# Kernel optimization log

Hardware: AMD Instinct MI355X
Metric: run time of the kernel (lower is better)

Reference implementation:

```python
import jax, jax.numpy as jnp
import numpy as np

DIM = 768
HEADS = 12
DIM_HEAD = DIM // HEADS  # 64
INNER = DIM_HEAD * HEADS  # 768
HIDDEN = 4 * DIM  # 3072
N = 31  # num_patches + 1, fixed by Block (num_patches=30)
B = 512
EPS = 1e-5
MASK_VAL = -987654321.0


def layernorm(x, g, b):
    mu = jnp.mean(x, axis=-1, keepdims=True)
    var = jnp.mean(jnp.square(x - mu), axis=-1, keepdims=True)
    return (x - mu) * jax.lax.rsqrt(var + EPS) * g + b


def setup_inputs() -> dict:
    key = jax.random.key(0)
    ks = jax.random.split(key, 12)
    s = 0.02
    return {
        "x": jax.random.normal(ks[0], (B, N, DIM), jnp.float32),
        "ln1_g": jnp.ones((DIM,), jnp.float32),
        "ln1_b": jnp.zeros((DIM,), jnp.float32),
        "w_qkv": jax.random.normal(ks[1], (DIM, 3 * INNER), jnp.float32) * s,
        "scale": jnp.full((HEADS,), DIM_HEAD ** -0.5, jnp.float32),
        "w_o": jax.random.normal(ks[2], (INNER, DIM), jnp.float32) * s,
        "b_o": jnp.zeros((DIM,), jnp.float32),
        "ln2_g": jnp.ones((DIM,), jnp.float32),
        "ln2_b": jnp.zeros((DIM,), jnp.float32),
        "w1": jax.random.normal(ks[3], (DIM, HIDDEN), jnp.float32) * s,
        "b1": jnp.zeros((HIDDEN,), jnp.float32),
        "w2": jax.random.normal(ks[4], (HIDDEN, DIM), jnp.float32) * s,
        "b2": jnp.zeros((DIM,), jnp.float32),
    }


def reference(x, ln1_g, ln1_b, w_qkv, scale, w_o, b_o, ln2_g, ln2_b, w1, b1, w2, b2):
    b, n, _ = x.shape
    # --- LSA attention ---
    h = layernorm(x, ln1_g, ln1_b)
    qkv = h @ w_qkv  # [b, n, 3*inner]
    q, k, v = jnp.split(qkv, 3, axis=-1)
    def split_heads(t):
        return t.reshape(b, n, HEADS, DIM_HEAD).transpose(0, 2, 1, 3)  # b h n d
    q, k, v = split_heads(q), split_heads(k), split_heads(v)
    dots = jnp.einsum('bhid,bhjd->bhij', q, k) * scale[None, :, None, None]
    # diagonal exclusion mask (self-token masked out)
    diag = jnp.eye(n, dtype=bool)
    dots = jnp.where(diag[None, None], MASK_VAL, dots)
    attn = jax.nn.softmax(dots, axis=-1)
    out = jnp.einsum('bhij,bhjd->bhid', attn, v)
    out = out.transpose(0, 2, 1, 3).reshape(b, n, INNER)
    x = x + out @ w_o + b_o
    # --- MLP ---
    h2 = layernorm(x, ln2_g, ln2_b)
    h2 = jax.nn.gelu(h2 @ w1 + b1, approximate=False)
    x = x + h2 @ w2 + b2
    return x
```

## Files before the change

### kernel.cpp

```cpp
#include <hip/hip_runtime.h>
#include <math.h>

#define DIM 768
#define HEADS 12
#define DHEAD 64
#define NTOK 31
#define BATCH 512
#define MTOK (BATCH * NTOK)
#define HIDDEN 3072
#define QKVN 2304
#define MASK_VAL -987654321.0f

typedef short s16x8 __attribute__((ext_vector_type(8)));
typedef float f32x4 __attribute__((ext_vector_type(4)));

static __device__ __forceinline__ float bs2f(unsigned short u) {
  unsigned int x = ((unsigned int)u) << 16;
  return __builtin_bit_cast(float, x);
}
static __device__ __forceinline__ unsigned short f2bs(float f) {
  unsigned int x = __builtin_bit_cast(unsigned int, f);
  x += 0x7fffu + ((x >> 16) & 1u);
  return (unsigned short)(x >> 16);
}

static __device__ __forceinline__ void gload16(const unsigned short* g, unsigned short* l) {
  __builtin_amdgcn_global_load_lds(
      (const __attribute__((address_space(1))) unsigned int*)g,
      (__attribute__((address_space(3))) unsigned int*)l, 16, 0, 0);
}

static __device__ __forceinline__ float epi_apply(int EPI, float v, int col, size_t idx,
                                                  const float* bias, const void* resid) {
  if (EPI == 0) return v;
  if (EPI == 2) {
    float t = v + bias[col];
    float arg = 1.5957691216f * t * (1.f + 0.044715f * t * t);
    return t * __builtin_amdgcn_rcpf(1.f + __expf(-arg));
  }
  if (EPI == 3) return v + bias[col] + ((const float*)resid)[idx];
  return v + bias[col] + bs2f(((const unsigned short*)resid)[idx]);
}

static __device__ __forceinline__ void epi_store(int EPI, void* outp, size_t idx, float t) {
  if (EPI == 4) ((float*)outp)[idx] = t;
  else ((unsigned short*)outp)[idx] = f2bs(t);
}

__global__ __launch_bounds__(256) void transpose_all_kernel(
    const float* __restrict__ w_qkv, const float* __restrict__ w_o,
    const float* __restrict__ w1, const float* __restrict__ w2,
    unsigned short* __restrict__ wqkvT, unsigned short* __restrict__ woT,
    unsigned short* __restrict__ w1T, unsigned short* __restrict__ w2T) {
  int t = blockIdx.x;
  const float* w;
  unsigned short* wt;
  int K, N, tx;
  if (t < 432) { w = w_qkv; wt = wqkvT; K = DIM; N = QKVN; tx = QKVN / 64; }
  else if (t < 576) { t -= 432; w = w_o; wt = woT; K = DIM; N = DIM; tx = DIM / 64; }
  else if (t < 1152) { t -= 576; w = w1; wt = w1T; K = DIM; N = HIDDEN; tx = HIDDEN / 64; }
  else { t -= 1152; w = w2; wt = w2T; K = HIDDEN; N = DIM; tx = DIM / 64; }
  int n0 = (t % tx) * 64, k0 = (t / tx) * 64;

  __shared__ float tl[64][65];
  int tid = threadIdx.x;
  int r = tid >> 4, c4 = (tid & 15) * 4;
#pragma unroll
  for (int i = 0; i < 4; ++i) {
    float4 v = *(const float4*)(w + (size_t)(k0 + r + i * 16) * N + n0 + c4);
    tl[r + i * 16][c4] = v.x;
    tl[r + i * 16][c4 + 1] = v.y;
    tl[r + i * 16][c4 + 2] = v.z;
    tl[r + i * 16][c4 + 3] = v.w;
  }
  __syncthreads();
#pragma unroll
  for (int i = 0; i < 4; ++i) {
    int n = r + i * 16;
    ushort4 o;
    o.x = f2bs(tl[c4 + 0][n]);
    o.y = f2bs(tl[c4 + 1][n]);
    o.z = f2bs(tl[c4 + 2][n]);
    o.w = f2bs(tl[c4 + 3][n]);
    *(ushort4*)(wt + (size_t)(n0 + n) * K + k0 + c4) = o;
  }
}

__global__ __launch_bounds__(256) void ln_kernel(const float* __restrict__ x,
                                                 const float* __restrict__ g,
                                                 const float* __restrict__ bta,
                                                 unsigned short* __restrict__ out) {
  int wid = threadIdx.x >> 6, lane = threadIdx.x & 63;
  size_t row = (size_t)blockIdx.x * 4 + wid;
  const float4* xr = (const float4*)(x + row * DIM);
  float4 v[3];
  v[0] = xr[lane];
  v[1] = xr[lane + 64];
  v[2] = xr[lane + 128];
  float s = 0.f, sq = 0.f;
#pragma unroll
  for (int i = 0; i < 3; ++i) {
    s += v[i].x + v[i].y + v[i].z + v[i].w;
    sq += v[i].x * v[i].x + v[i].y * v[i].y + v[i].z * v[i].z + v[i].w * v[i].w;
  }
#pragma unroll
  for (int off = 32; off; off >>= 1) {
    s += __shfl_xor(s, off);
    sq += __shfl_xor(sq, off);
  }
  float mu = s * (1.f / DIM);
  float var = sq * (1.f / DIM) - mu * mu;
  float rs = rsqrtf(var + 1e-5f);
#pragma unroll
  for (int i = 0; i < 3; ++i) {
    int col = i * 256 + lane * 4;
    float4 gg = *(const float4*)(g + col);
    float4 bb = *(const float4*)(bta + col);
    ushort4 o;
    o.x = f2bs((v[i].x - mu) * rs * gg.x + bb.x);
    o.y = f2bs((v[i].y - mu) * rs * gg.y + bb.y);
    o.z = f2bs((v[i].z - mu) * rs * gg.z + bb.z);
    o.w = f2bs((v[i].w - mu) * rs * gg.w + bb.w);
    *(ushort4*)(out + row * DIM + col) = o;
  }
}

__global__ __launch_bounds__(256) void ln_bf16_kernel(const unsigned short* __restrict__ x,
                                                      const float* __restrict__ g,
                                                      const float* __restrict__ bta,
                                                      unsigned short* __restrict__ out) {
  int wid = threadIdx.x >> 6, lane = threadIdx.x & 63;
  size_t row = (size_t)blockIdx.x * 4 + wid;
  const unsigned short* xr = x + row * DIM;
  float v[12];
#pragma unroll
  for (int i = 0; i < 3; ++i) {
    ushort4 u = *(const ushort4*)(xr + i * 256 + lane * 4);
    v[i * 4 + 0] = bs2f(u.x);
    v[i * 4 + 1] = bs2f(u.y);
    v[i * 4 + 2] = bs2f(u.z);
    v[i * 4 + 3] = bs2f(u.w);
  }
  float s = 0.f, sq = 0.f;
#pragma unroll
  for (int i = 0; i < 12; ++i) {
    s += v[i];
    sq += v[i] * v[i];
  }
#pragma unroll
  for (int off = 32; off; off >>= 1) {
    s += __shfl_xor(s, off);
    sq += __shfl_xor(sq, off);
  }
  float mu = s * (1.f / DIM);
  float var = sq * (1.f / DIM) - mu * mu;
  float rs = rsqrtf(var + 1e-5f);
#pragma unroll
  for (int i = 0; i < 3; ++i) {
    int col = i * 256 + lane * 4;
    float4 gg = *(const float4*)(g + col);
    float4 bb = *(const float4*)(bta + col);
    ushort4 o;
    o.x = f2bs((v[i * 4 + 0] - mu) * rs * gg.x + bb.x);
    o.y = f2bs((v[i * 4 + 1] - mu) * rs * gg.y + bb.y);
    o.z = f2bs((v[i * 4 + 2] - mu) * rs * gg.z + bb.z);
    o.w = f2bs((v[i * 4 + 3] - mu) * rs * gg.w + bb.w);
    *(ushort4*)(out + row * DIM + col) = o;
  }
}

template <int BUF, int MH, int KH, int VM, typename STF>
__device__ __forceinline__ void gph192(const char* aB0, const char* bKH0, const char* bKH1,
                                       s16x8 (&bk)[3], f32x4 (&acc)[8][3], STF&& stage) {
  const char* aP = aB0 + BUF * 32768 + KH * 16384 + MH * 4096;
  s16x8 af[4];
  if (MH == 0) {
    const char* bp = (KH ? bKH1 : bKH0) + BUF * 24576;
#pragma unroll
    for (int ni = 0; ni < 3; ++ni) bk[ni] = *(const s16x8*)(bp + ni * 2048);
  }
#pragma unroll
  for (int mi = 0; mi < 4; ++mi) af[mi] = *(const s16x8*)(aP + mi * 1024);
  stage();
  if (VM == 2) asm volatile("s_waitcnt vmcnt(2)");
  if (VM == 0) asm volatile("s_waitcnt vmcnt(0)");
  __builtin_amdgcn_s_barrier();
  asm volatile("s_waitcnt lgkmcnt(0)");
  __builtin_amdgcn_s_setprio(1);
#pragma unroll
  for (int mi = 0; mi < 4; ++mi)
#pragma unroll
    for (int ni = 0; ni < 3; ++ni)
      acc[MH * 4 + mi][ni] =
          __builtin_amdgcn_mfma_f32_16x16x32_bf16(af[mi], bk[ni], acc[MH * 4 + mi][ni], 0, 0, 0);
  __builtin_amdgcn_s_setprio(0);
  __builtin_amdgcn_s_barrier();
}

template <int EPI, int TPB>
__device__ __forceinline__ void gemm192_body(
    const unsigned short* __restrict__ A, const unsigned short* __restrict__ Bt,
    void* __restrict__ outp, const float* __restrict__ bias,
    const void* __restrict__ resid, int M, int N, int K, int ntn) {
  __shared__ char ldsc[114688];
  int tid = threadIdx.x;
  int lane = tid & 63, w = tid >> 6;
  int wm = w >> 2, wn = w & 3;
  int fr = lane & 15, q = lane >> 4;

  int nwg = gridDim.x, orig = blockIdx.x;
  int qd = nwg >> 3, r8 = nwg & 7, xcd = orig & 7, loc = orig >> 3;
  int bid = (xcd < r8 ? xcd * (qd + 1) : r8 * (qd + 1) + (xcd - r8) * qd) + loc;

  int rdoffA = (q * 16) ^ (((fr >> 1) & 3) << 4);
  const char* aB0 = ldsc + (wm * 128 + fr) * 64 + rdoffA;
  int brow0 = wn * 48 + fr;
  int bsw = brow0 & 7;
  const char* bBase = ldsc + 65536 + brow0 * 128 + (q ^ (bsw & 3)) * 16;
  const char* bKH0 = bBase + ((0 ^ (bsw >> 2)) * 64);
  const char* bKH1 = bBase + ((1 ^ (bsw >> 2)) * 64);

  int srow = tid >> 2;
  int seoffA = (((tid & 3) ^ ((srow >> 1) & 3))) << 3;
  size_t rstep = (size_t)K * 256;
  int NT = K / 64;

#pragma unroll 1
  for (int tl = 0; tl < TPB; ++tl) {
    int tile = bid * TPB + tl;
    int m0 = (tile / ntn) * 256, n0 = (tile % ntn) * 192;

    const char* Ab = (const char*)A + ((size_t)(m0 + srow) * K + seoffA) * 2;
    const char* Bb2 = (const char*)Bt +
        ((size_t)(n0 + (tid >> 3)) * K + (((tid & 7) ^ ((tid >> 3) & 7)) * 8)) * 2;

    auto stgA = [&](int kh, int buf, int t) {
      const char* gp = Ab + t * 128 + kh * 64;
      unsigned short* lp = (unsigned short*)(ldsc + buf * 32768 + kh * 16384 + w * 1024);
      gload16((const unsigned short*)gp, lp);
      gload16((const unsigned short*)(gp + rstep), (unsigned short*)((char*)lp + 8192));
    };
    auto stgB = [&](int j, int buf, int t) {
      gload16((const unsigned short*)(Bb2 + (size_t)j * 128 * K + t * 128),
              (unsigned short*)(ldsc + 65536 + buf * 24576 + j * 8192 + w * 1024));
    };
    auto nop = [&] {};

    f32x4 acc[8][3] = {};
    s16x8 bk[3];

    stgA(0, 0, 0);
    stgA(1, 0, 0);
    stgB(0, 0, 0);
    stgB(1, 0, 0);
    stgB(2, 0, 0);
    stgA(0, 1, 1);
    asm volatile("s_waitcnt vmcnt(2)");
    __builtin_amdgcn_s_barrier();

    for (int t = 0; t + 3 < NT; t += 2) {
      gph192<0, 0, 0, -1>(aB0, bKH0, bKH1, bk, acc,
                          [&] { stgA(1, 1, t + 1); stgB(0, 1, t + 1); stgB(1, 1, t + 1); });
      gph192<0, 1, 0, -1>(aB0, bKH0, bKH1, bk, acc, [&] { stgB(2, 1, t + 1); });
      gph192<0, 0, 1, -1>(aB0, bKH0, bKH1, bk, acc, [&] { stgA(0, 0, t + 2); });
      gph192<0, 1, 1, 2>(aB0, bKH0, bKH1, bk, acc, nop);
      gph192<1, 0, 0, -1>(aB0, bKH0, bKH1, bk, acc,
                          [&] { stgA(1, 0, t + 2); stgB(0, 0, t + 2); stgB(1, 0, t + 2); });
      gph192<1, 1, 0, -1>(aB0, bKH0, bKH1, bk, acc, [&] { stgB(2, 0, t + 2); });
      gph192<1, 0, 1, -1>(aB0, bKH0, bKH1, bk, acc, [&] { stgA(0, 1, t + 3); });
      gph192<1, 1, 1, 2>(aB0, bKH0, bKH1, bk, acc, nop);
    }
    gph192<0, 0, 0, -1>(aB0, bKH0, bKH1, bk, acc,
                        [&] { stgA(1, 1, NT - 1); stgB(0, 1, NT - 1); stgB(1, 1, NT - 1); });
    gph192<0, 1, 0, -1>(aB0, bKH0, bKH1, bk, acc, [&] { stgB(2, 1, NT - 1); });
    gph192<0, 0, 1, -1>(aB0, bKH0, bKH1, bk, acc, nop);
    gph192<0, 1, 1, 0>(aB0, bKH0, bKH1, bk, acc, nop);
    gph192<1, 0, 0, -1>(aB0, bKH0, bKH1, bk, acc, nop);
    gph192<1, 1, 0, -1>(aB0, bKH0, bKH1, bk, acc, nop);
    gph192<1, 0, 1, -1>(aB0, bKH0, bKH1, bk, acc, nop);
    gph192<1, 1, 1, -1>(aB0, bKH0, bKH1, bk, acc, nop);

#pragma unroll
    for (int am = 0; am < 8; ++am)
#pragma unroll
      for (int ni = 0; ni < 3; ++ni)
#pragma unroll
        for (int rr = 0; rr < 4; ++rr) {
          int row = m0 + wm * 128 + am * 16 + q * 4 + rr;
          int col = n0 + wn * 48 + ni * 16 + fr;
          size_t idx = (size_t)row * N + col;
          epi_store(EPI, outp, idx, epi_apply(EPI, acc[am][ni][rr], col, idx, bias, resid));
        }
  }
}

__global__ __launch_bounds__(512, 2) void gemm_qkv(const unsigned short* A,
                                                   const unsigned short* Bt, void* o,
                                                   const float* b, const void* r, int M,
                                                   int N, int K, int ntn) {
  gemm192_body<0, 3>(A, Bt, o, b, r, M, N, K, ntn);
}
__global__ __launch_bounds__(512, 2) void gemm_mlp1(const unsigned short* A,
                                                    const unsigned short* Bt, void* o,
                                                    const float* b, const void* r, int M,
                                                    int N, int K, int ntn) {
  gemm192_body<2, 4>(A, Bt, o, b, r, M, N, K, ntn);
}
__global__ __launch_bounds__(512, 2) void gemm_proj(const unsigned short* A,
                                                    const unsigned short* Bt, void* o,
                                                    const float* b, const void* r, int M,
                                                    int N, int K, int ntn) {
  gemm192_body<3, 1>(A, Bt, o, b, r, M, N, K, ntn);
}
__global__ __launch_bounds__(512, 2) void gemm_mlp2(const unsigned short* A,
                                                    const unsigned short* Bt, void* o,
                                                    const float* b, const void* r, int M,
                                                    int N, int K, int ntn) {
  gemm192_body<4, 1>(A, Bt, o, b, r, M, N, K, ntn);
}

__global__ __launch_bounds__(256) void attn_mfma_kernel(const unsigned short* __restrict__ qkv,
                                                        const float* __restrict__ scale,
                                                        unsigned short* __restrict__ ao) {
  __shared__ unsigned short Vt[4][64][40];
  __shared__ unsigned short Pl[4][32][32];
  int wid = threadIdx.x >> 6, lane = threadIdx.x & 63;
  int pair = blockIdx.x * 4 + wid;
  int b = pair / HEADS, h = pair % HEADS;
  const unsigned short* base = qkv + (size_t)b * NTOK * QKVN + h * DHEAD;
  const unsigned short* Qp = base;
  const unsigned short* Kp = base + 768;
  const unsigned short* Vp = base + 1536;

  int c = lane & 15, q = lane >> 4;
  int oct = q * 8;

  unsigned short vcol[NTOK];
#pragma unroll
  for (int j = 0; j < NTOK; ++j) vcol[j] = Vp[(size_t)j * QKVN + lane];
#pragma unroll
  for (int j = 0; j < NTOK; ++j) Vt[wid][lane][j] = vcol[j];
  Vt[wid][lane][31] = 0;

  s16x8 kf[2][2] = {{{0}}}, qf[2][2] = {{{0}}};
#pragma unroll
  for (int t = 0; t < 2; ++t) {
    int row = t * 16 + c;
    if (row < NTOK) {
#pragma unroll
      for (int s = 0; s < 2; ++s) {
        kf[t][s] = *(const s16x8*)(Kp + (size_t)row * QKVN + s * 32 + oct);
        qf[t][s] = *(const s16x8*)(Qp + (size_t)row * QKVN + s * 32 + oct);
      }
    }
  }

  f32x4 st[2][2] = {};
#pragma unroll
  for (int jt = 0; jt < 2; ++jt)
#pragma unroll
    for (int it = 0; it < 2; ++it)
#pragma unroll
      for (int s = 0; s < 2; ++s)
        st[jt][it] =
            __builtin_amdgcn_mfma_f32_16x16x32_bf16(kf[jt][s], qf[it][s], st[jt][it], 0, 0, 0);

  float scl = scale[h];
  float p[2][2][4];
#pragma unroll
  for (int it = 0; it < 2; ++it)
#pragma unroll
    for (int jt = 0; jt < 2; ++jt)
#pragma unroll
      for (int r = 0; r < 4; ++r) {
        int j = jt * 16 + 4 * q + r;
        int i = it * 16 + c;
        float v = st[jt][it][r] * scl;
        if (j == 31 || j == i) v = MASK_VAL;
        p[it][jt][r] = v;
      }
#pragma unroll
  for (int it = 0; it < 2; ++it) {
    float m = p[it][0][0];
#pragma unroll
    for (int jt = 0; jt < 2; ++jt)
#pragma unroll
      for (int r = 0; r < 4; ++r) m = fmaxf(m, p[it][jt][r]);
    m = fmaxf(m, __shfl_xor(m, 16));
    m = fmaxf(m, __shfl_xor(m, 32));
    float s = 0.f;
#pragma unroll
    for (int jt = 0; jt < 2; ++jt)
#pragma unroll
      for (int r = 0; r < 4; ++r) {
        float e = __expf(p[it][jt][r] - m);
        p[it][jt][r] = e;
        s += e;
      }
    s += __shfl_xor(s, 16);
    s += __shfl_xor(s, 32);
    float inv = __builtin_amdgcn_rcpf(s);
#pragma unroll
    for (int jt = 0; jt < 2; ++jt)
#pragma unroll
      for (int r = 0; r < 4; ++r) p[it][jt][r] *= inv;
  }
#pragma unroll
  for (int it = 0; it < 2; ++it)
#pragma unroll
    for (int jt = 0; jt < 2; ++jt) {
      unsigned int w0 =
          (unsigned int)f2bs(p[it][jt][0]) | ((unsigned int)f2bs(p[it][jt][1]) << 16);
      unsigned int w1 =
          (unsigned int)f2bs(p[it][jt][2]) | ((unsigned int)f2bs(p[it][jt][3]) << 16);
      uint2 pk = {w0, w1};
      *(uint2*)&Pl[wid][it * 16 + c][jt * 16 + 4 * q] = pk;
    }

  s16x8 pa[2];
#pragma unroll
  for (int it = 0; it < 2; ++it) pa[it] = *(const s16x8*)&Pl[wid][it * 16 + c][oct];
  f32x4 o[2][4];
#pragma unroll
  for (int it = 0; it < 2; ++it)
#pragma unroll
    for (int dt = 0; dt < 4; ++dt) {
      s16x8 vb = *(const s16x8*)&Vt[wid][dt * 16 + c][oct];
      f32x4 z = {0.f, 0.f, 0.f, 0.f};
      o[it][dt] = __builtin_amdgcn_mfma_f32_16x16x32_bf16(pa[it], vb, z, 0, 0, 0);
    }
#pragma unroll
  for (int it = 0; it < 2; ++it)
#pragma unroll
    for (int r = 0; r < 4; ++r) {
      int i = it * 16 + 4 * q + r;
      if (i < NTOK) {
        size_t rowoff = ((size_t)b * NTOK + i) * DIM + h * DHEAD;
#pragma unroll
        for (int dt = 0; dt < 4; ++dt) ao[rowoff + dt * 16 + c] = f2bs(o[it][dt][r]);
      }
    }
}

extern "C" void kernel_launch(void* const* d_in, const int* in_sizes, int n_in,
                              void* d_out, int out_size, void* d_ws, size_t ws_size,
                              hipStream_t stream) {
  (void)in_sizes; (void)n_in; (void)out_size; (void)ws_size;
  const float* x = (const float*)d_in[0];
  const float* ln1_g = (const float*)d_in[1];
  const float* ln1_b = (const float*)d_in[2];
  const float* w_qkv = (const float*)d_in[3];
  const float* scale = (const float*)d_in[4];
  const float* w_o = (const float*)d_in[5];
  const float* b_o = (const float*)d_in[6];
  const float* ln2_g = (const float*)d_in[7];
  const float* ln2_b = (const float*)d_in[8];
  const float* w1 = (const float*)d_in[9];
  const float* b1 = (const float*)d_in[10];
  const float* w2 = (const float*)d_in[11];
  const float* b2 = (const float*)d_in[12];

  char* ws = (char*)d_ws;
  unsigned short* buf1 = (unsigned short*)(ws + 0);
  unsigned short* qkv_bf = (unsigned short*)(ws + 24379392);
  unsigned short* x2 = (unsigned short*)(ws + 24379392);
  unsigned short* g_bf = (unsigned short*)(ws + 97517568);
  unsigned short* wqkvT = (unsigned short*)(ws + 195035136);
  unsigned short* woT = (unsigned short*)(ws + 198574080);
  unsigned short* w1T = (unsigned short*)(ws + 199753728);
  unsigned short* w2T = (unsigned short*)(ws + 204472320);

  transpose_all_kernel<<<1728, 256, 0, stream>>>(w_qkv, w_o, w1, w2, wqkvT, woT, w1T, w2T);

  ln_kernel<<<MTOK / 4, 256, 0, stream>>>(x, ln1_g, ln1_b, buf1);
  gemm_qkv<<<248, 512, 0, stream>>>(
      buf1, wqkvT, qkv_bf, nullptr, nullptr, MTOK, QKVN, DIM, QKVN / 192);
  attn_mfma_kernel<<<(BATCH * HEADS) / 4, 256, 0, stream>>>(qkv_bf, scale, buf1);
  gemm_proj<<<248, 512, 0, stream>>>(
      buf1, woT, x2, b_o, x, MTOK, DIM, DIM, DIM / 192);
  ln_bf16_kernel<<<MTOK / 4, 256, 0, stream>>>(x2, ln2_g, ln2_b, buf1);
  gemm_mlp1<<<248, 512, 0, stream>>>(
      buf1, w1T, g_bf, b1, nullptr, MTOK, HIDDEN, DIM, HIDDEN / 192);
  gemm_mlp2<<<248, 512, 0, stream>>>(
      g_bf, w2T, (float*)d_out, b2, x2, MTOK, DIM, HIDDEN, DIM / 192);
}
```

Measured before the change: 313.2 us.

## Double-buffer LDS fragment reads to overlap with MFMA in 192-wide GEMM

Each GEMM phase now prefetches the next phase's A and B fragments from LDS into a second register buffer right after the barrier. It then issues the MFMAs on the current buffer instead of waiting on lgkmcnt for its own fragments. This hides LDS read latency behind the matrix ops. It costs extra VGPRs for the doubled fragment arrays, which could cause spills at launch bounds of 512 threads and 2 blocks. It also relies on the compiler inserting the correct lgkmcnt waits.

```diff
diff --git a/kernel.cpp b/kernel.cpp
--- a/kernel.cpp
+++ b/kernel.cpp
@@ -169,30 +169,32 @@
   }
 }
 
-template <int BUF, int MH, int KH, int VM, typename STF>
-__device__ __forceinline__ void gph192(const char* aB0, const char* bKH0, const char* bKH1,
-                                       s16x8 (&bk)[3], f32x4 (&acc)[8][3], STF&& stage) {
-  const char* aP = aB0 + BUF * 32768 + KH * 16384 + MH * 4096;
-  s16x8 af[4];
-  if (MH == 0) {
-    const char* bp = (KH ? bKH1 : bKH0) + BUF * 24576;
-#pragma unroll
-    for (int ni = 0; ni < 3; ++ni) bk[ni] = *(const s16x8*)(bp + ni * 2048);
-  }
-#pragma unroll
-  for (int mi = 0; mi < 4; ++mi) af[mi] = *(const s16x8*)(aP + mi * 1024);
+template <int CMH, int CS, int CB, int RBUF, int RMH, int RKH, int RB, int VM, int NORD,
+          typename STF>
+__device__ __forceinline__ void gphP(const char* aB0, const char* bKH0, const char* bKH1,
+                                     s16x8 (&af2)[2][4], s16x8 (&bk2)[2][3],
+                                     f32x4 (&acc)[8][3], STF&& stage) {
   stage();
   if (VM == 2) asm volatile("s_waitcnt vmcnt(2)");
   if (VM == 0) asm volatile("s_waitcnt vmcnt(0)");
   __builtin_amdgcn_s_barrier();
-  asm volatile("s_waitcnt lgkmcnt(0)");
+  if (!NORD) {
+    const char* aP = aB0 + RBUF * 32768 + RKH * 16384 + RMH * 4096;
+#pragma unroll
+    for (int mi = 0; mi < 4; ++mi) af2[CS ^ 1][mi] = *(const s16x8*)(aP + mi * 1024);
+    if (RMH == 0) {
+      const char* bp = (RKH ? bKH1 : bKH0) + RBUF * 24576;
+#pragma unroll
+      for (int ni = 0; ni < 3; ++ni) bk2[RB][ni] = *(const s16x8*)(bp + ni * 2048);
+    }
+  }
   __builtin_amdgcn_s_setprio(1);
 #pragma unroll
   for (int mi = 0; mi < 4; ++mi)
 #pragma unroll
     for (int ni = 0; ni < 3; ++ni)
-      acc[MH * 4 + mi][ni] =
-          __builtin_amdgcn_mfma_f32_16x16x32_bf16(af[mi], bk[ni], acc[MH * 4 + mi][ni], 0, 0, 0);
+      acc[CMH * 4 + mi][ni] = __builtin_amdgcn_mfma_f32_16x16x32_bf16(
+          af2[CS][mi], bk2[CB][ni], acc[CMH * 4 + mi][ni], 0, 0, 0);
   __builtin_amdgcn_s_setprio(0);
   __builtin_amdgcn_s_barrier();
 }
@@ -247,7 +249,7 @@
     auto nop = [&] {};
 
     f32x4 acc[8][3] = {};
-    s16x8 bk[3];
+    s16x8 af2[2][4], bk2[2][3];
 
     stgA(0, 0, 0);
     stgA(1, 0, 0);
@@ -257,28 +259,39 @@
     stgA(0, 1, 1);
     asm volatile("s_waitcnt vmcnt(2)");
     __builtin_amdgcn_s_barrier();
+    {
+#pragma unroll
+      for (int mi = 0; mi < 4; ++mi) af2[0][mi] = *(const s16x8*)(aB0 + mi * 1024);
+#pragma unroll
+      for (int ni = 0; ni < 3; ++ni) bk2[0][ni] = *(const s16x8*)(bKH0 + ni * 2048);
+    }
 
     for (int t = 0; t + 3 < NT; t += 2) {
-      gph192<0, 0, 0, -1>(aB0, bKH0, bKH1, bk, acc,
-                          [&] { stgA(1, 1, t + 1); stgB(0, 1, t + 1); stgB(1, 1, t + 1); });
-      gph192<0, 1, 0, -1>(aB0, bKH0, bKH1, bk, acc, [&] { stgB(2, 1, t + 1); });
-      gph192<0, 0, 1, -1>(aB0, bKH0, bKH1, bk, acc, [&] { stgA(0, 0, t + 2); });
-      gph192<0, 1, 1, 2>(aB0, bKH0, bKH1, bk, acc, nop);
-      gph192<1, 0, 0, -1>(aB0, bKH0, bKH1, bk, acc,
-                          [&] { stgA(1, 0, t + 2); stgB(0, 0, t + 2); stgB(1, 0, t + 2); });
-      gph192<1, 1, 0, -1>(aB0, bKH0, bKH1, bk, acc, [&] { stgB(2, 0, t + 2); });
-      gph192<1, 0, 1, -1>(aB0, bKH0, bKH1, bk, acc, [&] { stgA(0, 1, t + 3); });
-      gph192<1, 1, 1, 2>(aB0, bKH0, bKH1, bk, acc, nop);
-    }
-    gph192<0, 0, 0, -1>(aB0, bKH0, bKH1, bk, acc,
-                        [&] { stgA(1, 1, NT - 1); stgB(0, 1, NT - 1); stgB(1, 1, NT - 1); });
-    gph192<0, 1, 0, -1>(aB0, bKH0, bKH1, bk, acc, [&] { stgB(2, 1, NT - 1); });
-    gph192<0, 0, 1, -1>(aB0, bKH0, bKH1, bk, acc, nop);
-    gph192<0, 1, 1, 0>(aB0, bKH0, bKH1, bk, acc, nop);
-    gph192<1, 0, 0, -1>(aB0, bKH0, bKH1, bk, acc, nop);
-    gph192<1, 1, 0, -1>(aB0, bKH0, bKH1, bk, acc, nop);
-    gph192<1, 0, 1, -1>(aB0, bKH0, bKH1, bk, acc, nop);
-    gph192<1, 1, 1, -1>(aB0, bKH0, bKH1, bk, acc, nop);
+      gphP<0, 0, 0, 0, 1, 0, 0, -1, 0>(aB0, bKH0, bKH1, af2, bk2, acc,
+          [&] { stgA(1, 1, t + 1); stgB(0, 1, t + 1); stgB(1, 1, t + 1); });
+      gphP<1, 1, 0, 0, 0, 1, 1, -1, 0>(aB0, bKH0, bKH1, af2, bk2, acc,
+          [&] { stgB(2, 1, t + 1); });
+      gphP<0, 0, 1, 0, 1, 1, 0, -1, 0>(aB0, bKH0, bKH1, af2, bk2, acc,
+          [&] { stgA(0, 0, t + 2); });
+      gphP<1, 1, 1, 1, 0, 0, 0, 2, 0>(aB0, bKH0, bKH1, af2, bk2, acc, nop);
+      gphP<0, 0, 0, 1, 1, 0, 0, -1, 0>(aB0, bKH0, bKH1, af2, bk2, acc,
+          [&] { stgA(1, 0, t + 2); stgB(0, 0, t + 2); stgB(1, 0, t + 2); });
+      gphP<1, 1, 0, 1, 0, 1, 1, -1, 0>(aB0, bKH0, bKH1, af2, bk2, acc,
+          [&] { stgB(2, 0, t + 2); });
+      gphP<0, 0, 1, 1, 1, 1, 0, -1, 0>(aB0, bKH0, bKH1, af2, bk2, acc,
+          [&] { stgA(0, 1, t + 3); });
+      gphP<1, 1, 1, 0, 0, 0, 0, 2, 0>(aB0, bKH0, bKH1, af2, bk2, acc, nop);
+    }
+    gphP<0, 0, 0, 0, 1, 0, 0, -1, 0>(aB0, bKH0, bKH1, af2, bk2, acc,
+        [&] { stgA(1, 1, NT - 1); stgB(0, 1, NT - 1); stgB(1, 1, NT - 1); });
+    gphP<1, 1, 0, 0, 0, 1, 1, -1, 0>(aB0, bKH0, bKH1, af2, bk2, acc,
+        [&] { stgB(2, 1, NT - 1); });
+    gphP<0, 0, 1, 0, 1, 1, 0, -1, 0>(aB0, bKH0, bKH1, af2, bk2, acc, nop);
+    gphP<1, 1, 1, 1, 0, 0, 0, 0, 0>(aB0, bKH0, bKH1, af2, bk2, acc, nop);
+    gphP<0, 0, 0, 1, 1, 0, 0, -1, 0>(aB0, bKH0, bKH1, af2, bk2, acc, nop);
+    gphP<1, 1, 0, 1, 0, 1, 1, -1, 0>(aB0, bKH0, bKH1, af2, bk2, acc, nop);
+    gphP<0, 0, 1, 1, 1, 1, 0, -1, 0>(aB0, bKH0, bKH1, af2, bk2, acc, nop);
+    gphP<1, 1, 1, 0, 0, 0, 0, -1, 1>(aB0, bKH0, bKH1, af2, bk2, acc, nop);
 
 #pragma unroll
     for (int am = 0; am < 8; ++am)
```

Result: no change. 310.4 us (-0.9%).
